# Kernel tuning notes

Hardware: AMD Instinct MI355X
Metric: run time of the kernel (lower is better)

The kernel has to match this reference:

```python
import jax, jax.numpy as jnp
from jax import lax
import numpy as np

NUM_STEPS = 20
GATE_TIME = 1.0
DT = GATE_TIME / NUM_STEPS
BATCH = 8388608  # number of qubit states (columns)


def setup_inputs() -> dict:
    key = jax.random.key(0)
    k1, k2 = jax.random.split(key)
    # learnable pulse amplitudes, initialized to 2.0 as in the torch module
    amplitudes = jnp.full((NUM_STEPS,), 2.0, dtype=jnp.float32)
    state_real = jax.random.normal(k1, (2, BATCH), dtype=jnp.float32)
    state_imag = jax.random.normal(k2, (2, BATCH), dtype=jnp.float32)
    return {"amplitudes": amplitudes, "state_real": state_real, "state_imag": state_imag}


def reference(amplitudes, state_real, state_imag):
    # H_k = (a_k / 2) * X ;  U_k = exp(-i * H_k * dt) = cos(a_k*dt/2) I - i sin(a_k*dt/2) X
    # (exact closed form of matrix_exp for the Pauli-X generator)
    state = state_real + 1j * state_imag  # [2, B] complex64

    def step(s, a):
        theta = a * (DT * 0.5)
        c = jnp.cos(theta)
        sn = jnp.sin(theta)
        # X @ s swaps the two rows
        s_new = c * s - 1j * sn * s[::-1, :]
        return s_new, None

    state, _ = lax.scan(step, state, amplitudes)
    # return real-valued view [2(real/imag), 2, B]
    return jnp.stack([state.real, state.imag])
```

## Files before the change

kernel.cpp:

```cpp
#include <hip/hip_runtime.h>


typedef float f4 __attribute__((ext_vector_type(4)));

__global__ __launch_bounds__(256) void grape_kernel(
    const float* __restrict__ amps, int nsteps,
    const float* __restrict__ sreal, const float* __restrict__ simag,
    float* __restrict__ out, long long B) {
    float theta = 0.0f;
    for (int k = 0; k < nsteps; ++k) theta += amps[k];
    theta *= (1.0f / (float)nsteps) * 0.5f;
    float c = cosf(theta);
    float s = sinf(theta);

    long long idx = (long long)blockIdx.x * blockDim.x + threadIdx.x;
    long long j = idx * 4;

    if (j + 3 < B) {
        const f4 r0 = *(const f4*)(sreal + j);
        const f4 r1 = *(const f4*)(sreal + B + j);
        const f4 i0 = *(const f4*)(simag + j);
        const f4 i1 = *(const f4*)(simag + B + j);

        const f4 or0 = c * r0 + s * i1;
        const f4 or1 = c * r1 + s * i0;
        const f4 oi0 = c * i0 - s * r1;
        const f4 oi1 = c * i1 - s * r0;

        __builtin_nontemporal_store(or0, (f4*)(out + j));
        __builtin_nontemporal_store(or1, (f4*)(out + B + j));
        __builtin_nontemporal_store(oi0, (f4*)(out + 2 * B + j));
        __builtin_nontemporal_store(oi1, (f4*)(out + 3 * B + j));
    } else if (j < B) {
        for (long long t = j; t < B; ++t) {
            float r0 = sreal[t], r1 = sreal[B + t];
            float i0 = simag[t], i1 = simag[B + t];
            __builtin_nontemporal_store(c * r0 + s * i1, out + t);
            __builtin_nontemporal_store(c * r1 + s * i0, out + B + t);
            __builtin_nontemporal_store(c * i0 - s * r1, out + 2 * B + t);
            __builtin_nontemporal_store(c * i1 - s * r0, out + 3 * B + t);
        }
    }
}

extern "C" void kernel_launch(void* const* d_in, const int* in_sizes, int n_in,
                              void* d_out, int out_size, void* d_ws, size_t ws_size,
                              hipStream_t stream) {
    const float* amps  = (const float*)d_in[0];
    const float* sreal = (const float*)d_in[1];
    const float* simag = (const float*)d_in[2];
    float* out = (float*)d_out;

    int nsteps = in_sizes[0];
    long long B = (long long)in_sizes[1] / 2;

    long long nthreads = (B + 3) / 4;
    int block = 256;
    long long grid = (nthreads + block - 1) / block;

    grape_kernel<<<(dim3)(unsigned)grid, block, 0, stream>>>(
        amps, nsteps, sreal, simag, out, B);
}
```

Baseline: 245.7 us.

## Use grid-stride loop with 8 floats per thread and regular stores

```diff
diff --git a/kernel.cpp b/kernel.cpp
--- a/kernel.cpp
+++ b/kernel.cpp
@@ -10,36 +10,45 @@
     float theta = 0.0f;
     for (int k = 0; k < nsteps; ++k) theta += amps[k];
     theta *= (1.0f / (float)nsteps) * 0.5f;
-    float c = cosf(theta);
-    float s = sinf(theta);
+    const float c = cosf(theta);
+    const float s = sinf(theta);
 
-    long long idx = (long long)blockIdx.x * blockDim.x + threadIdx.x;
-    long long j = idx * 4;
+    const long long nv = B >> 3;
+    const long long stride = (long long)gridDim.x * blockDim.x;
 
-    if (j + 3 < B) {
-        const f4 r0 = *(const f4*)(sreal + j);
-        const f4 r1 = *(const f4*)(sreal + B + j);
-        const f4 i0 = *(const f4*)(simag + j);
-        const f4 i1 = *(const f4*)(simag + B + j);
+    for (long long v = (long long)blockIdx.x * blockDim.x + threadIdx.x;
+         v < nv; v += stride) {
+        const long long j = v << 3;
 
-        const f4 or0 = c * r0 + s * i1;
-        const f4 or1 = c * r1 + s * i0;
-        const f4 oi0 = c * i0 - s * r1;
-        const f4 oi1 = c * i1 - s * r0;
+        const f4 r0a = *(const f4*)(sreal + j);
+        const f4 r0b = *(const f4*)(sreal + j + 4);
+        const f4 r1a = *(const f4*)(sreal + B + j);
+        const f4 r1b = *(const f4*)(sreal + B + j + 4);
+        const f4 i0a = *(const f4*)(simag + j);
+        const f4 i0b = *(const f4*)(simag + j + 4);
+        const f4 i1a = *(const f4*)(simag + B + j);
+        const f4 i1b = *(const f4*)(simag + B + j + 4);
 
-        __builtin_nontemporal_store(or0, (f4*)(out + j));
-        __builtin_nontemporal_store(or1, (f4*)(out + B + j));
-        __builtin_nontemporal_store(oi0, (f4*)(out + 2 * B + j));
-        __builtin_nontemporal_store(oi1, (f4*)(out + 3 * B + j));
-    } else if (j < B) {
-        for (long long t = j; t < B; ++t) {
-            float r0 = sreal[t], r1 = sreal[B + t];
-            float i0 = simag[t], i1 = simag[B + t];
-            __builtin_nontemporal_store(c * r0 + s * i1, out + t);
-            __builtin_nontemporal_store(c * r1 + s * i0, out + B + t);
-            __builtin_nontemporal_store(c * i0 - s * r1, out + 2 * B + t);
-            __builtin_nontemporal_store(c * i1 - s * r0, out + 3 * B + t);
-        }
+        *(f4*)(out + j)             = c * r0a + s * i1a;
+        *(f4*)(out + j + 4)         = c * r0b + s * i1b;
+        *(f4*)(out + B + j)         = c * r1a + s * i0a;
+        *(f4*)(out + B + j + 4)     = c * r1b + s * i0b;
+        *(f4*)(out + 2 * B + j)     = c * i0a - s * r1a;
+        *(f4*)(out + 2 * B + j + 4) = c * i0b - s * r1b;
+        *(f4*)(out + 3 * B + j)     = c * i1a - s * r0a;
+        *(f4*)(out + 3 * B + j + 4) = c * i1b - s * r0b;
+    }
+
+    const long long tail_start = nv << 3;
+    const long long t =
+        tail_start + (long long)blockIdx.x * blockDim.x + threadIdx.x;
+    if (t < B) {
+        const float r0 = sreal[t], r1 = sreal[B + t];
+        const float i0 = simag[t], i1 = simag[B + t];
+        out[t]         = c * r0 + s * i1;
+        out[B + t]     = c * r1 + s * i0;
+        out[2 * B + t] = c * i0 - s * r1;
+        out[3 * B + t] = c * i1 - s * r0;
     }
 }
 
@@ -54,9 +63,11 @@
     int nsteps = in_sizes[0];
     long long B = (long long)in_sizes[1] / 2;
 
-    long long nthreads = (B + 3) / 4;
-    int block = 256;
-    long long grid = (nthreads + block - 1) / block;
+    const int block = 256;
+    long long nv = B >> 3;
+    long long grid = (nv + block - 1) / block;
+    if (grid > 2048) grid = 2048;
+    if (grid < 1) grid = 1;
 
     grape_kernel<<<(dim3)(unsigned)grid, block, 0, stream>>>(
         amps, nsteps, sreal, simag, out, B);
```

Result: no change. 244.1 us (-0.7%).
